# Performance work log

Measured on AMD Instinct MI355X. Metric: run time of the kernel, lower is better.

## Reference

```python
import jax, jax.numpy as jnp
import numpy as np

B, N, DIM = 4, 8192, 512
HEADS, DIM_HEAD = 8, 64
INNER = HEADS * DIM_HEAD          # 512
M = DIM // 2                      # 256 landmarks
PINV_ITERS = 6
RES_K = 33                        # residual depthwise conv kernel (default in NystromAttention)
LN_EPS = 1e-5


def setup_inputs() -> dict:
    key = jax.random.key(0)
    ks = jax.random.split(key, 5)
    s = 0.02
    return {
        "x": jax.random.normal(ks[0], (B, N, DIM), jnp.float32),
        "ln_w": jnp.ones((DIM,), jnp.float32),
        "ln_b": jnp.zeros((DIM,), jnp.float32),
        "w_qkv": jax.random.normal(ks[1], (DIM, 3 * INNER), jnp.float32) * s,
        "w_out": jax.random.normal(ks[2], (INNER, DIM), jnp.float32) * s,
        "b_out": jnp.zeros((DIM,), jnp.float32),
        "res_w": jax.random.normal(ks[3], (HEADS, RES_K), jnp.float32) * s,
    }


def _moore_penrose_pinv(x, iters=PINV_ITERS):
    # Newton-Schulz iteration, exactly as in nystrom-attention
    abs_x = jnp.abs(x)
    col = abs_x.sum(axis=-1)
    row = abs_x.sum(axis=-2)
    z = jnp.swapaxes(x, -1, -2) / (jnp.max(col) * jnp.max(row))
    I = jnp.eye(x.shape[-1], dtype=x.dtype)
    for _ in range(iters):
        xz = x @ z
        z = 0.25 * z @ (13.0 * I - xz @ (15.0 * I - xz @ (7.0 * I - xz)))
    return z


def reference(x, ln_w, ln_b, w_qkv, w_out, b_out, res_w):
    b, n, d = x.shape
    # --- LayerNorm (biased variance, eps=1e-5) ---
    mu = x.mean(-1, keepdims=True)
    var = ((x - mu) ** 2).mean(-1, keepdims=True)
    xn = (x - mu) * jax.lax.rsqrt(var + LN_EPS) * ln_w + ln_b

    # --- pad on the LEFT so seq len divisible by num_landmarks ---
    pad = (-n) % M
    xp = jnp.pad(xn, ((0, 0), (pad, 0), (0, 0)))
    n_p = n + pad

    # --- qkv projection, split heads ---
    qkv = xp @ w_qkv                                  # [b, n_p, 3*inner]
    q, k, v = jnp.split(qkv, 3, axis=-1)
    to_h = lambda t: t.reshape(b, n_p, HEADS, DIM_HEAD).transpose(0, 2, 1, 3)
    q, k, v = to_h(q), to_h(k), to_h(v)               # [b, h, n_p, dh]
    q = q * (DIM_HEAD ** -0.5)

    # --- landmarks: mean over contiguous groups ---
    l = n_p // M
    q_l = q.reshape(b, HEADS, M, l, DIM_HEAD).mean(axis=3)   # [b, h, m, dh]
    k_l = k.reshape(b, HEADS, M, l, DIM_HEAD).mean(axis=3)

    # --- three similarity matrices + softmaxes ---
    sim1 = jnp.einsum('bhnd,bhmd->bhnm', q, k_l)      # [b,h,n_p,m]
    sim2 = jnp.einsum('bhmd,bhld->bhml', q_l, k_l)    # [b,h,m,m]
    sim3 = jnp.einsum('bhmd,bhnd->bhmn', q_l, k)      # [b,h,m,n_p]
    attn1 = jax.nn.softmax(sim1, axis=-1)
    attn2 = jax.nn.softmax(sim2, axis=-1)
    attn3 = jax.nn.softmax(sim3, axis=-1)

    attn2_inv = _moore_penrose_pinv(attn2)
    out = (attn1 @ attn2_inv) @ (attn3 @ v)           # [b,h,n_p,dh]

    # --- residual depthwise conv over sequence dim (groups = heads) ---
    kern = res_w[:, None, :, None]                    # [h, 1, 33, 1] OIHW
    res = jax.lax.conv_general_dilated(
        v, kern, window_strides=(1, 1),
        padding=((RES_K // 2, RES_K // 2), (0, 0)),
        dimension_numbers=('NCHW', 'OIHW', 'NCHW'),
        feature_group_count=HEADS)
    out = out + res

    # --- merge heads, output projection, strip padding, residual add ---
    out = out.transpose(0, 2, 1, 3).reshape(b, n_p, INNER)
    out = out @ w_out + b_out
    out = out[:, -n:]
    return x + out
```

## Files before the change

kernel.cpp:

```cpp
#include <hip/hip_runtime.h>
#include <cstdint>

#define B_ 4
#define N_ 8192
#define DIM_ 512
#define H_ 8
#define DH_ 64
#define M_ 256
#define L_ 32
#define INNER_ 512
#define K3_ 1536
#define RESK_ 33

struct __align__(16) ushort8_t { unsigned short u[8]; };
typedef short bf16x8 __attribute__((ext_vector_type(8)));
typedef float f32x4 __attribute__((ext_vector_type(4)));

__device__ __forceinline__ float bf2f(unsigned short u) {
  return __uint_as_float(((unsigned)u) << 16);
}
__device__ __forceinline__ unsigned short f2bf(float f) {
  unsigned x = __float_as_uint(f);
  return (unsigned short)((x + 0x7fffu + ((x >> 16) & 1u)) >> 16);
}

__global__ __launch_bounds__(256) void ln_bf16(const float* __restrict__ x,
    const float* __restrict__ w, const float* __restrict__ bb, unsigned short* __restrict__ xnb)
{
  int row = blockIdx.x;
  int tid = threadIdx.x;
  float2 v = reinterpret_cast<const float2*>(x + (size_t)row * DIM_)[tid];
  float s = v.x + v.y, s2 = v.x * v.x + v.y * v.y;
  #pragma unroll
  for (int off = 32; off; off >>= 1) { s += __shfl_down(s, off); s2 += __shfl_down(s2, off); }
  __shared__ float rs[4], rs2[4];
  int wid = tid >> 6, lane = tid & 63;
  if (lane == 0) { rs[wid] = s; rs2[wid] = s2; }
  __syncthreads();
  float ts = rs[0] + rs[1] + rs[2] + rs[3];
  float ts2 = rs2[0] + rs2[1] + rs2[2] + rs2[3];
  float mu = ts * (1.f / DIM_);
  float var = ts2 * (1.f / DIM_) - mu * mu;
  float inv = rsqrtf(var + 1e-5f);
  int c = tid * 2;
  unsigned int p0 = f2bf((v.x - mu) * inv * w[c] + bb[c]);
  unsigned int p1 = f2bf((v.y - mu) * inv * w[c + 1] + bb[c + 1]);
  reinterpret_cast<unsigned int*>(xnb + (size_t)row * DIM_)[tid] = p0 | (p1 << 16);
}

__global__ __launch_bounds__(256) void transpose_w(const float* __restrict__ src,
    unsigned short* __restrict__ dst, int K, int C, int qcols, float qs)
{
  __shared__ float T[64][65];
  int c0 = blockIdx.x * 64, k0 = blockIdx.y * 64;
  #pragma unroll 4
  for (int it = 0; it < 16; it++) {
    int idx = it * 256 + threadIdx.x;
    int kk = idx >> 6, cc = idx & 63;
    T[kk][cc] = src[(size_t)(k0 + kk) * C + c0 + cc];
  }
  __syncthreads();
  #pragma unroll 4
  for (int it = 0; it < 16; it++) {
    int idx = it * 256 + threadIdx.x;
    int cc = idx >> 6, kk = idx & 63;
    float v = T[kk][cc];
    int c = c0 + cc;
    dst[(size_t)c * K + k0 + kk] = f2bf(c < qcols ? v * qs : v);
  }
}

__global__ __launch_bounds__(256, 2) void mfma_qkv(const unsigned short* __restrict__ xnb,
    const unsigned short* __restrict__ wT,
    unsigned short* __restrict__ qb, unsigned short* __restrict__ kb, unsigned short* __restrict__ vb)
{
  __shared__ unsigned short As[128][72];
  __shared__ unsigned short Bs[128][72];
  int tid = threadIdx.x;
  int bn = blockIdx.x * 128, bm = blockIdx.y * 128;
  int wid = tid >> 6, lane = tid & 63;
  int wr = wid >> 1, wc = wid & 1;
  int lr = lane & 15, lg = lane >> 4;
  const f32x4 zf = {0.f, 0.f, 0.f, 0.f};
  f32x4 acc[4][4];
  #pragma unroll
  for (int mt = 0; mt < 4; mt++)
    #pragma unroll
    for (int nt = 0; nt < 4; nt++) acc[mt][nt] = zf;

  for (int k0 = 0; k0 < DIM_; k0 += 64) {
    __syncthreads();
    #pragma unroll
    for (int rnd = 0; rnd < 4; rnd++) {
      int idx = rnd * 2048 + tid * 8;
      int row = idx >> 6, col = idx & 63;
      *reinterpret_cast<bf16x8*>(&As[row][col]) =
          *reinterpret_cast<const bf16x8*>(&xnb[(size_t)(bm + row) * DIM_ + k0 + col]);
      *reinterpret_cast<bf16x8*>(&Bs[row][col]) =
          *reinterpret_cast<const bf16x8*>(&wT[(size_t)(bn + row) * DIM_ + k0 + col]);
    }
    __syncthreads();
    bf16x8 af[4][2], bfr[4][2];
    #pragma unroll
    for (int mt = 0; mt < 4; mt++) {
      af[mt][0] = *reinterpret_cast<const bf16x8*>(&As[wr * 64 + mt * 16 + lr][lg * 8]);
      af[mt][1] = *reinterpret_cast<const bf16x8*>(&As[wr * 64 + mt * 16 + lr][32 + lg * 8]);
    }
    #pragma unroll
    for (int nt = 0; nt < 4; nt++) {
      bfr[nt][0] = *reinterpret_cast<const bf16x8*>(&Bs[wc * 64 + nt * 16 + lr][lg * 8]);
      bfr[nt][1] = *reinterpret_cast<const bf16x8*>(&Bs[wc * 64 + nt * 16 + lr][32 + lg * 8]);
    }
    #pragma unroll
    for (int mt = 0; mt < 4; mt++)
      #pragma unroll
      for (int nt = 0; nt < 4; nt++) {
        acc[mt][nt] = __builtin_amdgcn_mfma_f32_16x16x32_bf16(af[mt][0], bfr[nt][0], acc[mt][nt], 0, 0, 0);
        acc[mt][nt] = __builtin_amdgcn_mfma_f32_16x16x32_bf16(af[mt][1], bfr[nt][1], acc[mt][nt], 0, 0, 0);
      }
  }
  #pragma unroll
  for (int nt = 0; nt < 4; nt++) {
    int c = bn + wc * 64 + nt * 16 + lr;
    int which = c >> 9;
    int h = (c >> 6) & (H_ - 1);
    int d = c & 63;
    unsigned short* dst = which == 0 ? qb : (which == 1 ? kb : vb);
    #pragma unroll
    for (int mt = 0; mt < 4; mt++)
      #pragma unroll
      for (int r = 0; r < 4; r++) {
        int row = bm + wr * 64 + mt * 16 + 4 * lg + r;
        int b = row >> 13, n = row & (N_ - 1);
        dst[(((size_t)(b * H_ + h) * N_ + n) << 6) + d] = f2bf(acc[mt][nt][r]);
      }
  }
}

__global__ __launch_bounds__(256, 2) void mfma_out(const unsigned short* __restrict__ oh,
    const unsigned short* __restrict__ wT, const float* __restrict__ bias,
    const float* __restrict__ resid, float* __restrict__ out)
{
  __shared__ unsigned short As[128][72];
  __shared__ unsigned short Bs[128][72];
  int tid = threadIdx.x;
  int bn = blockIdx.x * 128, bm = blockIdx.y * 128;
  int wid = tid >> 6, lane = tid & 63;
  int wr = wid >> 1, wc = wid & 1;
  int lr = lane & 15, lg = lane >> 4;
  const f32x4 zf = {0.f, 0.f, 0.f, 0.f};
  f32x4 acc[4][4];
  #pragma unroll
  for (int mt = 0; mt < 4; mt++)
    #pragma unroll
    for (int nt = 0; nt < 4; nt++) acc[mt][nt] = zf;

  for (int k0 = 0; k0 < INNER_; k0 += 64) {
    __syncthreads();
    #pragma unroll
    for (int rnd = 0; rnd < 4; rnd++) {
      int idx = rnd * 2048 + tid * 8;
      int row = idx >> 6, col = idx & 63;
      *reinterpret_cast<bf16x8*>(&As[row][col]) =
          *reinterpret_cast<const bf16x8*>(&oh[((size_t)(bm + row) << 9) + k0 + col]);
      *reinterpret_cast<bf16x8*>(&Bs[row][col]) =
          *reinterpret_cast<const bf16x8*>(&wT[(size_t)(bn + row) * INNER_ + k0 + col]);
    }
    __syncthreads();
    bf16x8 af[4][2], bfr[4][2];
    #pragma unroll
    for (int mt = 0; mt < 4; mt++) {
      af[mt][0] = *reinterpret_cast<const bf16x8*>(&As[wr * 64 + mt * 16 + lr][lg * 8]);
      af[mt][1] = *reinterpret_cast<const bf16x8*>(&As[wr * 64 + mt * 16 + lr][32 + lg * 8]);
    }
    #pragma unroll
    for (int nt = 0; nt < 4; nt++) {
      bfr[nt][0] = *reinterpret_cast<const bf16x8*>(&Bs[wc * 64 + nt * 16 + lr][lg * 8]);
      bfr[nt][1] = *reinterpret_cast<const bf16x8*>(&Bs[wc * 64 + nt * 16 + lr][32 + lg * 8]);
    }
    #pragma unroll
    for (int mt = 0; mt < 4; mt++)
      #pragma unroll
      for (int nt = 0; nt < 4; nt++) {
        acc[mt][nt] = __builtin_amdgcn_mfma_f32_16x16x32_bf16(af[mt][0], bfr[nt][0], acc[mt][nt], 0, 0, 0);
        acc[mt][nt] = __builtin_amdgcn_mfma_f32_16x16x32_bf16(af[mt][1], bfr[nt][1], acc[mt][nt], 0, 0, 0);
      }
  }
  #pragma unroll
  for (int nt = 0; nt < 4; nt++) {
    int c = bn + wc * 64 + nt * 16 + lr;
    float bias_c = bias[c];
    #pragma unroll
    for (int mt = 0; mt < 4; mt++)
      #pragma unroll
      for (int r = 0; r < 4; r++) {
        int row = bm + wr * 64 + mt * 16 + 4 * lg + r;
        out[(size_t)row * DIM_ + c] = acc[mt][nt][r] + bias_c + resid[(size_t)row * DIM_ + c];
      }
  }
}

__global__ __launch_bounds__(64) void landmark_kernel(const unsigned short* __restrict__ qb,
    const unsigned short* __restrict__ kb, float* __restrict__ ql, float* __restrict__ kl,
    unsigned short* __restrict__ qlb, unsigned short* __restrict__ klb)
{
  int id = blockIdx.x;
  int m = id & (M_ - 1);
  int bh = id >> 8;
  int d = threadIdx.x;
  size_t base = (((size_t)bh * N_ + m * L_) << 6) + d;
  float sq = 0, sk = 0;
  #pragma unroll 4
  for (int j = 0; j < L_; j++) {
    sq += bf2f(qb[base + ((size_t)j << 6)]);
    sk += bf2f(kb[base + ((size_t)j << 6)]);
  }
  float qv = sq * (1.f / L_);
  float kv = sk * (1.f / L_);
  size_t o = ((size_t)bh * M_ + m) * DH_ + d;
  ql[o] = qv;
  kl[o] = kv;
  qlb[o] = f2bf(qv);
  klb[o] = f2bf(kv);
}

__global__ __launch_bounds__(256) void attn2_kernel(const float* __restrict__ ql,
    const float* __restrict__ kl, float* __restrict__ a2, unsigned short* __restrict__ a2b)
{
  int id = blockIdx.x;
  int i = id & (M_ - 1);
  int bh = id >> 8;
  int j = threadIdx.x;
  __shared__ float qs[DH_];
  __shared__ float wred[4];
  if (j < DH_) qs[j] = ql[((size_t)bh * M_ + i) * DH_ + j];
  __syncthreads();
  const float* krow = kl + ((size_t)bh * M_ + j) * DH_;
  float s = 0;
  #pragma unroll
  for (int d = 0; d < DH_; d++) s += qs[d] * krow[d];
  float mx = s;
  #pragma unroll
  for (int off = 1; off < 64; off <<= 1) mx = fmaxf(mx, __shfl_xor(mx, off));
  int wid = j >> 6, lane = j & 63;
  if (lane == 0) wred[wid] = mx;
  __syncthreads();
  mx = fmaxf(fmaxf(wred[0], wred[1]), fmaxf(wred[2], wred[3]));
  float e = __expf(s - mx);
  float sum = e;
  #pragma unroll
  for (int off = 1; off < 64; off <<= 1) sum += __shfl_xor(sum, off);
  __syncthreads();
  if (lane == 0) wred[wid] = sum;
  __syncthreads();
  sum = wred[0] + wred[1] + wred[2] + wred[3];
  float p = e / sum;
  size_t o = ((size_t)bh * M_ + i) * M_ + j;
  a2[o] = p;
  a2b[o] = f2bf(p);
}

__global__ void zero_scal(unsigned int* scal) { scal[threadIdx.x] = 0u; }

__global__ __launch_bounds__(256) void pinv_scale_kernel(const float* __restrict__ a2,
    unsigned int* __restrict__ scal)
{
  int bh = blockIdx.x;
  int t = threadIdx.x;
  const float* xb = a2 + (size_t)bh * M_ * M_;
  float rowsum = 0, colsum = 0;
  for (int j = 0; j < M_; j++) {
    rowsum += xb[(size_t)t * M_ + j];
    colsum += xb[(size_t)j * M_ + t];
  }
  #pragma unroll
  for (int off = 1; off < 64; off <<= 1) {
    rowsum = fmaxf(rowsum, __shfl_xor(rowsum, off));
    colsum = fmaxf(colsum, __shfl_xor(colsum, off));
  }
  __shared__ float wr[4], wc[4];
  int wid = t >> 6, lane = t & 63;
  if (lane == 0) { wr[wid] = rowsum; wc[wid] = colsum; }
  __syncthreads();
  if (t == 0) {
    float rm = fmaxf(fmaxf(wr[0], wr[1]), fmaxf(wr[2], wr[3]));
    float cm = fmaxf(fmaxf(wc[0], wc[1]), fmaxf(wc[2], wc[3]));
    atomicMax(&scal[0], __float_as_uint(rm));
    atomicMax(&scal[1], __float_as_uint(cm));
  }
}

__global__ __launch_bounds__(256) void zinit_kernel(const float* __restrict__ a2,
    const unsigned int* __restrict__ scal,
    unsigned short* __restrict__ zR, unsigned short* __restrict__ zT)
{
  __shared__ float T[64][65];
  int j0 = blockIdx.x * 64, i0 = blockIdx.y * 64;
  size_t bb = (size_t)blockIdx.z * (M_ * M_);
  float inv = 1.f / (__uint_as_float(scal[0]) * __uint_as_float(scal[1]));
  int tid = threadIdx.x;
  #pragma unroll 4
  for (int pass = 0; pass < 16; pass++) {
    int idx = pass * 256 + tid;
    int ii = idx >> 6, jj = idx & 63;
    float v = a2[bb + (size_t)(i0 + ii) * M_ + j0 + jj];
    T[ii][jj] = v;
    zT[bb + (size_t)(i0 + ii) * M_ + j0 + jj] = f2bf(v * inv);
  }
  __syncthreads();
  #pragma unroll 4
  for (int pass = 0; pass < 16; pass++) {
    int idx = pass * 256 + tid;
    int jj = idx >> 6, ii = idx & 63;
    zR[bb + (size_t)(j0 + jj) * M_ + i0 + ii] = f2bf(T[ii][jj] * inv);
  }
}

__global__ __launch_bounds__(256, 2) void bgemm_ns(
    const unsigned short* __restrict__ Ab, const unsigned short* __restrict__ BTb,
    unsigned short* __restrict__ Rb, unsigned short* __restrict__ YTb,
    float aY, float sY, float sR)
{
  __shared__ unsigned short Ash[64][72];
  __shared__ unsigned short Bsh[64][72];
  int bn = blockIdx.x * 64, bm = blockIdx.y * 64;
  size_t bb = (size_t)blockIdx.z * (M_ * M_);
  int tid = threadIdx.x, wid = tid >> 6, lane = tid & 63;
  int lr = lane & 15, lg = lane >> 4;
  int wr = (wid >> 1) * 32, wc = (wid & 1) * 32;
  const f32x4 zf = {0.f, 0.f, 0.f, 0.f};
  f32x4 acc[2][2];
  #pragma unroll
  for (int mt = 0; mt < 2; mt++)
    #pragma unroll
    for (int nt = 0; nt < 2; nt++) acc[mt][nt] = zf;

  for (int k0 = 0; k0 < M_; k0 += 64) {
    __syncthreads();
    #pragma unroll
    for (int pass = 0; pass < 2; pass++) {
      int idx = pass * 2048 + tid * 8;
      int row = idx >> 6, col = idx & 63;
      *reinterpret_cast<bf16x8*>(&Ash[row][col]) =
          *reinterpret_cast<const bf16x8*>(&Ab[bb + (size_t)(bm + row) * M_ + k0 + col]);
      *reinterpret_cast<bf16x8*>(&Bsh[row][col]) =
          *reinterpret_cast<const bf16x8*>(&BTb[bb + (size_t)(bn + row) * M_ + k0 + col]);
    }
    __syncthreads();
    #pragma unroll
    for (int kk = 0; kk < 64; kk += 32) {
      bf16x8 a0 = *reinterpret_cast<const bf16x8*>(&Ash[wr + lr][kk + lg * 8]);
      bf16x8 a1 = *reinterpret_cast<const bf16x8*>(&Ash[wr + 16 + lr][kk + lg * 8]);
      bf16x8 b0 = *reinterpret_cast<const bf16x8*>(&Bsh[wc + lr][kk + lg * 8]);
      bf16x8 b1 = *reinterpret_cast<const bf16x8*>(&Bsh[wc + 16 + lr][kk + lg * 8]);
      acc[0][0] = __builtin_amdgcn_mfma_f32_16x16x32_bf16(a0, b0, acc[0][0], 0, 0, 0);
      acc[0][1] = __builtin_amdgcn_mfma_f32_16x16x32_bf16(a0, b1, acc[0][1], 0, 0, 0);
      acc[1][0] = __builtin_amdgcn_mfma_f32_16x16x32_bf16(a1, b0, acc[1][0], 0, 0, 0);
      acc[1][1] = __builtin_amdgcn_mfma_f32_16x16x32_bf16(a1, b1, acc[1][1], 0, 0, 0);
    }
  }
  if (Rb) {
    #pragma unroll
    for (int mt = 0; mt < 2; mt++)
      #pragma unroll
      for (int nt = 0; nt < 2; nt++) {
        int col = bn + wc + nt * 16 + lr;
        #pragma unroll
        for (int r = 0; r < 4; r++) {
          int row = bm + wr + mt * 16 + 4 * lg + r;
          Rb[bb + (size_t)row * M_ + col] = f2bf(sR * acc[mt][nt][r]);
        }
      }
  }
  if (YTb) {
    __syncthreads();
    #pragma unroll
    for (int mt = 0; mt < 2; mt++)
      #pragma unroll
      for (int nt = 0; nt < 2; nt++) {
        int nl = wc + nt * 16 + lr;
        #pragma unroll
        for (int r = 0; r < 4; r++) {
          int ml = wr + mt * 16 + 4 * lg + r;
          float t = sY * acc[mt][nt][r] + ((bm + ml) == (bn + nl) ? aY : 0.f);
          Ash[nl][ml] = f2bf(t);
        }
      }
    __syncthreads();
    #pragma unroll
    for (int pass = 0; pass < 2; pass++) {
      int idx = pass * 2048 + tid * 8;
      int nl = idx >> 6, ml = idx & 63;
      *reinterpret_cast<bf16x8*>(&YTb[bb + (size_t)(bn + nl) * M_ + bm + ml]) =
          *reinterpret_cast<const bf16x8*>(&Ash[nl][ml]);
    }
  }
}

__global__ __launch_bounds__(256) void gemm_w2(
    const unsigned short* __restrict__ zR,
    const unsigned short* __restrict__ pvT, unsigned short* __restrict__ w2t)
{
  int bm = blockIdx.x * 64;
  int batch = blockIdx.y;
  size_t bz = (size_t)batch * (M_ * M_);
  size_t bp = (size_t)batch << 14;
  int tid = threadIdx.x, wid = tid >> 6, lane = tid & 63;
  int lr = lane & 15, lg = lane >> 4;
  int r0 = bm + wid * 16;
  const f32x4 zf = {0.f, 0.f, 0.f, 0.f};
  f32x4 acc[4];
  #pragma unroll
  for (int nt = 0; nt < 4; nt++) acc[nt] = zf;

  #pragma unroll
  for (int k0 = 0; k0 < M_; k0 += 32) {
    bf16x8 a = *reinterpret_cast<const bf16x8*>(&zR[bz + (size_t)(r0 + lr) * M_ + k0 + lg * 8]);
    #pragma unroll
    for (int nt = 0; nt < 4; nt++) {
      bf16x8 b = *reinterpret_cast<const bf16x8*>(&pvT[bp + (size_t)(nt * 16 + lr) * M_ + k0 + lg * 8]);
      acc[nt] = __builtin_amdgcn_mfma_f32_16x16x32_bf16(a, b, acc[nt], 0, 0, 0);
    }
  }
  #pragma unroll
  for (int nt = 0; nt < 4; nt++) {
    int col = nt * 16 + lr;
    #pragma unroll
    for (int r = 0; r < 4; r++) {
      int row = r0 + 4 * lg + r;
      w2t[bp + (size_t)col * M_ + row] = f2bf(acc[nt][r]);
    }
  }
}

__global__ __launch_bounds__(512) void pv_mfma(
    const unsigned short* __restrict__ kb, const unsigned short* __restrict__ vb,
    const unsigned short* __restrict__ qlb,
    float* __restrict__ pvpart, float2* __restrict__ msbuf)
{
  int slice = blockIdx.x;
  int bh    = blockIdx.z;
  int tid = threadIdx.x, wid = tid >> 6, lane = tid & 63;
  int lr = lane & 15, lg = lane >> 4;

  __shared__ unsigned short klds[64][72];
  __shared__ unsigned short vtld[64][72];
  __shared__ unsigned short plds_all[8][32][72];
  unsigned short (*plds)[72] = plds_all[wid];

  int mbase = wid * 32;
  const unsigned short* qbase = qlb + (((size_t)bh * M_ + mbase) << 6);
  bf16x8 qf[2][2];
  #pragma unroll
  for (int rt = 0; rt < 2; rt++)
    #pragma unroll
    for (int h2 = 0; h2 < 2; h2++)
      qf[rt][h2] = *reinterpret_cast<const bf16x8*>(&qbase[((rt * 16 + lr) << 6) + h2 * 32 + lg * 8]);

  const f32x4 zf = {0.f, 0.f, 0.f, 0.f};
  f32x4 oacc[2][4];
  #pragma unroll
  for (int rt = 0; rt < 2; rt++)
    #pragma unroll
    for (int dt = 0; dt < 4; dt++) oacc[rt][dt] = zf;
  float mrun[8], srun[8];
  #pragma unroll
  for (int i = 0; i < 8; i++) { mrun[i] = -1e30f; srun[i] = 0.f; }

  const unsigned short* kgb = kb + (((size_t)bh * N_ + slice * 1024) << 6);
  const unsigned short* vgb = vb + (((size_t)bh * N_ + slice * 1024) << 6);

  for (int c = 0; c < 16; c++) {
    __syncthreads();
    {
      int key = tid >> 3, seg = tid & 7;
      size_t goff = (((size_t)(c * 64 + key)) << 6) + seg * 8;
      bf16x8 kv = *reinterpret_cast<const bf16x8*>(&kgb[goff]);
      *reinterpret_cast<bf16x8*>(&klds[key][seg * 8]) = kv;
      bf16x8 vv = *reinterpret_cast<const bf16x8*>(&vgb[goff]);
      int col = key ^ (seg << 3);
      #pragma unroll
      for (int j = 0; j < 8; j++) vtld[seg * 8 + j][col] = (unsigned short)vv[j];
    }
    __syncthreads();
    f32x4 sacc[2][4];
    #pragma unroll
    for (int rt = 0; rt < 2; rt++)
      #pragma unroll
      for (int ct = 0; ct < 4; ct++) {
        bf16x8 b0 = *reinterpret_cast<const bf16x8*>(&klds[ct * 16 + lr][lg * 8]);
        bf16x8 b1 = *reinterpret_cast<const bf16x8*>(&klds[ct * 16 + lr][32 + lg * 8]);
        f32x4 a = __builtin_amdgcn_mfma_f32_16x16x32_bf16(qf[rt][0], b0, zf, 0, 0, 0);
        sacc[rt][ct] = __builtin_amdgcn_mfma_f32_16x16x32_bf16(qf[rt][1], b1, a, 0, 0, 0);
      }
    #pragma unroll
    for (int rt = 0; rt < 2; rt++)
      #pragma unroll
      for (int r = 0; r < 4; r++) {
        int ri = rt * 4 + r;
        float mc = fmaxf(fmaxf(sacc[rt][0][r], sacc[rt][1][r]), fmaxf(sacc[rt][2][r], sacc[rt][3][r]));
        #pragma unroll
        for (int off = 1; off < 16; off <<= 1) mc = fmaxf(mc, __shfl_xor(mc, off));
        float mnew = fmaxf(mrun[ri], mc);
        float corr = __expf(mrun[ri] - mnew);
        float psum = 0.f;
        #pragma unroll
        for (int ct = 0; ct < 4; ct++) {
          float p = __expf(sacc[rt][ct][r] - mnew);
          sacc[rt][ct][r] = p;
          psum += p;
        }
        #pragma unroll
        for (int off = 1; off < 16; off <<= 1) psum += __shfl_xor(psum, off);
        srun[ri] = srun[ri] * corr + psum;
        mrun[ri] = mnew;
        #pragma unroll
        for (int dt = 0; dt < 4; dt++) oacc[rt][dt][r] *= corr;
        #pragma unroll
        for (int ct = 0; ct < 4; ct++)
          plds[rt * 16 + 4 * lg + r][ct * 16 + lr] = f2bf(sacc[rt][ct][r]);
      }
    __builtin_amdgcn_s_waitcnt(0);
    bf16x8 pa[2][2];
    #pragma unroll
    for (int rt = 0; rt < 2; rt++)
      #pragma unroll
      for (int h = 0; h < 2; h++)
        pa[rt][h] = *reinterpret_cast<const bf16x8*>(&plds[rt * 16 + lr][h * 32 + lg * 8]);
    #pragma unroll
    for (int dt = 0; dt < 4; dt++) {
      int d = dt * 16 + lr;
      bf16x8 bv0 = *reinterpret_cast<const bf16x8*>(&vtld[d][(lg * 8) ^ (d & 0x38)]);
      bf16x8 bv1 = *reinterpret_cast<const bf16x8*>(&vtld[d][(32 + lg * 8) ^ (d & 0x38)]);
      #pragma unroll
      for (int rt = 0; rt < 2; rt++) {
        oacc[rt][dt] = __builtin_amdgcn_mfma_f32_16x16x32_bf16(pa[rt][0], bv0, oacc[rt][dt], 0, 0, 0);
        oacc[rt][dt] = __builtin_amdgcn_mfma_f32_16x16x32_bf16(pa[rt][1], bv1, oacc[rt][dt], 0, 0, 0);
      }
    }
  }
  size_t pbase = (((size_t)(bh * 8 + slice) * M_ + mbase) << 6);
  #pragma unroll
  for (int rt = 0; rt < 2; rt++)
    #pragma unroll
    for (int dt = 0; dt < 4; dt++)
      #pragma unroll
      for (int r = 0; r < 4; r++)
        pvpart[pbase + ((size_t)(rt * 16 + 4 * lg + r) << 6) + dt * 16 + lr] = oacc[rt][dt][r];
  if (lr == 0) {
    #pragma unroll
    for (int rt = 0; rt < 2; rt++)
      #pragma unroll
      for (int r = 0; r < 4; r++)
        msbuf[(size_t)(bh * 8 + slice) * M_ + mbase + rt * 16 + 4 * lg + r] =
            make_float2(mrun[rt * 4 + r], srun[rt * 4 + r]);
  }
}

__global__ __launch_bounds__(256) void pv_combine(const float* __restrict__ pvpart,
    const float2* __restrict__ msbuf, unsigned short* __restrict__ pvT)
{
  int row = blockIdx.x * 4 + (threadIdx.x >> 6);
  int bh = row >> 8, m = row & (M_ - 1);
  int d = threadIdx.x & 63;
  float2 ms[8];
  float mg = -1e30f;
  #pragma unroll
  for (int s = 0; s < 8; s++) {
    ms[s] = msbuf[(size_t)(bh * 8 + s) * M_ + m];
    mg = fmaxf(mg, ms[s].x);
  }
  float ssum = 0.f, o = 0.f;
  #pragma unroll
  for (int s = 0; s < 8; s++) {
    float w = __expf(ms[s].x - mg);
    ssum += ms[s].y * w;
    o += w * pvpart[(((size_t)(bh * 8 + s) * M_ + m) << 6) + d];
  }
  pvT[((size_t)bh << 14) + (size_t)d * M_ + m] = f2bf(o / ssum);
}

__global__ __launch_bounds__(256) void attn1_kernel(
    const unsigned short* __restrict__ qb,
    const unsigned short* __restrict__ klb,
    const unsigned short* __restrict__ w2t,
    unsigned short* __restrict__ oh)
{
  int ntile = blockIdx.x & 31;
  int bh = blockIdx.x >> 5;
  int h = bh & (H_ - 1), b = bh >> 3;
  int tid = threadIdx.x, wid = tid >> 6, lane = tid & 63;
  int lr = lane & 15, lg = lane >> 4;
  __shared__ unsigned short klds[256][72];
  __shared__ unsigned short plds_all[4][16][264];
  unsigned short* plds = &plds_all[wid][0][0];

  const unsigned short* qbh  = qb  + (((size_t)bh * N_) << 6);
  const unsigned short* klbh = klb + ((size_t)bh << 14);
  const unsigned short* w2bh = w2t + ((size_t)bh << 14);

  #pragma unroll
  for (int e = 0; e < 8; e++) {
    int idx = e * 2048 + tid * 8;
    int row = idx >> 6, col = idx & 63;
    *reinterpret_cast<bf16x8*>(&klds[row][col]) =
        *reinterpret_cast<const bf16x8*>(&klbh[((size_t)row << 6) + col]);
  }
  __syncthreads();

  const f32x4 zf = {0.f, 0.f, 0.f, 0.f};
  for (int sub = 0; sub < 4; sub++) {
    int n0 = ntile * 256 + sub * 64 + wid * 16;
    bf16x8 aq0 = *reinterpret_cast<const bf16x8*>(&qbh[((size_t)(n0 + lr) << 6) + lg * 8]);
    bf16x8 aq1 = *reinterpret_cast<const bf16x8*>(&qbh[((size_t)(n0 + lr) << 6) + 32 + lg * 8]);
    f32x4 accs[16];
    #pragma unroll
    for (int mt = 0; mt < 16; mt++) {
      bf16x8 b0 = *reinterpret_cast<const bf16x8*>(&klds[mt * 16 + lr][lg * 8]);
      bf16x8 b1 = *reinterpret_cast<const bf16x8*>(&klds[mt * 16 + lr][32 + lg * 8]);
      f32x4 a = __builtin_amdgcn_mfma_f32_16x16x32_bf16(aq0, b0, zf, 0, 0, 0);
      accs[mt] = __builtin_amdgcn_mfma_f32_16x16x32_bf16(aq1, b1, a, 0, 0, 0);
    }
    float rs[4];
    #pragma unroll
    for (int r = 0; r < 4; r++) {
      float m0 = accs[0][r];
      #pragma unroll
      for (int mt = 1; mt < 16; mt++) m0 = fmaxf(m0, accs[mt][r]);
      #pragma unroll
      for (int off = 1; off < 16; off <<= 1) m0 = fmaxf(m0, __shfl_xor(m0, off));
      float s0 = 0.f;
      #pragma unroll
      for (int mt = 0; mt < 16; mt++) {
        float p = __expf(accs[mt][r] - m0);
        accs[mt][r] = p;
        s0 += p;
      }
      #pragma unroll
      for (int off = 1; off < 16; off <<= 1) s0 += __shfl_xor(s0, off);
      rs[r] = 1.f / s0;
    }
    #pragma unroll
    for (int mt = 0; mt < 16; mt++)
      #pragma unroll
      for (int r = 0; r < 4; r++)
        plds[(4 * lg + r) * 264 + mt * 16 + lr] = f2bf(accs[mt][r]);
    __builtin_amdgcn_s_waitcnt(0);
    bf16x8 pa[8];
    #pragma unroll
    for (int mc = 0; mc < 8; mc++)
      pa[mc] = *reinterpret_cast<const bf16x8*>(&plds[lr * 264 + mc * 32 + lg * 8]);
    f32x4 acco[4];
    #pragma unroll
    for (int dt = 0; dt < 4; dt++) {
      f32x4 a = zf;
      #pragma unroll
      for (int mc = 0; mc < 8; mc++) {
        bf16x8 wf = *reinterpret_cast<const bf16x8*>(&w2bh[(size_t)(dt * 16 + lr) * M_ + mc * 32 + lg * 8]);
        a = __builtin_amdgcn_mfma_f32_16x16x32_bf16(pa[mc], wf, a, 0, 0, 0);
      }
      acco[dt] = a;
    }
    #pragma unroll
    for (int dt = 0; dt < 4; dt++)
      #pragma unroll
      for (int r = 0; r < 4; r++) {
        int n = n0 + 4 * lg + r;
        oh[((size_t)(b * N_ + n) << 9) + h * DH_ + dt * 16 + lr] = f2bf(acco[dt][r] * rs[r]);
      }
  }
}

__global__ __launch_bounds__(256) void conv_kernel(const unsigned short* __restrict__ vb,
    const float* __restrict__ rw, unsigned short* __restrict__ oh)
{
  int bh = blockIdx.y;
  int h = bh & (H_ - 1), b = bh >> 3;
  int d = threadIdx.x & 63, g = threadIdx.x >> 6;
  int n0 = blockIdx.x * 128 + g * 32;
  const unsigned short* vbb = vb + (((size_t)bh * N_) << 6) + d;
  float w[64];
  #pragma unroll
  for (int j = 0; j < 64; j++) {
    int nn = n0 - 16 + j;
    w[j] = (nn >= 0 && nn < N_) ? bf2f(vbb[(size_t)nn << 6]) : 0.f;
  }
  float rwr[RESK_];
  #pragma unroll
  for (int j = 0; j < RESK_; j++) rwr[j] = rw[h * RESK_ + j];
  size_t obase = (((size_t)(b * N_ + n0)) << 9) + h * 64 + d;
  #pragma unroll
  for (int t = 0; t < 32; t++) {
    float acc = 0.f;
    #pragma unroll
    for (int j = 0; j < RESK_; j++) acc += rwr[j] * w[t + j];
    size_t oi = obase + ((size_t)t << 9);
    oh[oi] = f2bf(bf2f(oh[oi]) + acc);
  }
}

extern "C" void kernel_launch(void* const* d_in, const int* in_sizes, int n_in,
                              void* d_out, int out_size, void* d_ws, size_t ws_size,
                              hipStream_t stream)
{
  const float* x     = (const float*)d_in[0];
  const float* ln_w  = (const float*)d_in[1];
  const float* ln_b  = (const float*)d_in[2];
  const float* w_qkv = (const float*)d_in[3];
  const float* w_out = (const float*)d_in[4];
  const float* b_out = (const float*)d_in[5];
  const float* res_w = (const float*)d_in[6];
  float* out = (float*)d_out;

  const size_t HEADEL = (size_t)B_ * H_ * N_ * DH_;
  const size_t SMALL  = (size_t)B_ * H_ * M_ * DH_;
  const size_t MSQ    = (size_t)B_ * H_ * M_ * M_;

  char* p = (char*)d_ws;
  auto alloc = [&](size_t bytes) { char* r = p; p += (bytes + 255) & ~(size_t)255; return r; };

  unsigned short* qb  = (unsigned short*)alloc(HEADEL * 2);
  unsigned short* kb  = (unsigned short*)alloc(HEADEL * 2);
  unsigned short* vb  = (unsigned short*)alloc(HEADEL * 2);
  unsigned short* oh  = (unsigned short*)alloc(HEADEL * 2);
  char* unA = alloc(HEADEL * 2);
  unsigned short* xnb = (unsigned short*)unA;
  unsigned short* z0R = (unsigned short*)unA;
  unsigned short* z0T = z0R + MSQ;
  unsigned short* z1R = z0T + MSQ;
  unsigned short* z1T = z1R + MSQ;
  char* unB = alloc(HEADEL * 2);
  float*  pvpart = (float*)unB;
  float2* msbuf  = (float2*)(unB + (size_t)B_ * H_ * 8 * M_ * DH_ * 4);
  unsigned short* ub  = (unsigned short*)unB;
  unsigned short* vTb = ub + MSQ;
  unsigned short* wTb = vTb + MSQ;
  unsigned short* yTb = wTb + MSQ;

  unsigned short* wqkvT = (unsigned short*)alloc((size_t)K3_ * DIM_ * 2);
  unsigned short* woutT = (unsigned short*)alloc((size_t)DIM_ * INNER_ * 2);
  float* ql  = (float*)alloc(SMALL * 4);
  float* kl  = (float*)alloc(SMALL * 4);
  unsigned short* qlb = (unsigned short*)alloc(SMALL * 2);
  unsigned short* klb = (unsigned short*)alloc(SMALL * 2);
  unsigned short* pvT = (unsigned short*)alloc(SMALL * 2);
  unsigned short* w2t = (unsigned short*)alloc(SMALL * 2);
  unsigned short* a2b = (unsigned short*)alloc(MSQ * 2);
  unsigned int* scal  = (unsigned int*)alloc(256);
  if ((size_t)(p - (char*)d_ws) > ws_size) return;

  float* a2 = (float*)d_out;

  ln_bf16<<<B_ * N_, 256, 0, stream>>>(x, ln_w, ln_b, xnb);
  transpose_w<<<dim3(K3_ / 64, DIM_ / 64), 256, 0, stream>>>(w_qkv, wqkvT, DIM_, K3_, INNER_, 0.125f);
  transpose_w<<<dim3(DIM_ / 64, INNER_ / 64), 256, 0, stream>>>(w_out, woutT, INNER_, DIM_, 0, 1.f);
  mfma_qkv<<<dim3(K3_ / 128, (B_ * N_) / 128), 256, 0, stream>>>(xnb, wqkvT, qb, kb, vb);
  landmark_kernel<<<B_ * H_ * M_, 64, 0, stream>>>(qb, kb, ql, kl, qlb, klb);
  attn2_kernel<<<B_ * H_ * M_, 256, 0, stream>>>(ql, kl, a2, a2b);
  zero_scal<<<1, 2, 0, stream>>>(scal);
  pinv_scale_kernel<<<B_ * H_, 256, 0, stream>>>(a2, scal);
  pv_mfma<<<dim3(8, 1, B_ * H_), 512, 0, stream>>>(kb, vb, qlb, pvpart, msbuf);
  pv_combine<<<(B_ * H_ * M_) / 4, 256, 0, stream>>>(pvpart, msbuf, pvT);
  zinit_kernel<<<dim3(4, 4, B_ * H_), 256, 0, stream>>>(a2, scal, z0R, z0T);

  unsigned short *cR = z0R, *cT = z0T, *nR = z1R, *nT = z1T;
  dim3 g44(4, 4, B_ * H_);
  for (int it = 0; it < 6; it++) {
    bgemm_ns<<<g44, 256, 0, stream>>>(a2b, cT, ub, vTb, 7.f, -1.f, 1.f);
    bgemm_ns<<<g44, 256, 0, stream>>>(ub, vTb, nullptr, wTb, 15.f, -1.f, 0.f);
    bgemm_ns<<<g44, 256, 0, stream>>>(ub, wTb, nullptr, yTb, 13.f, -1.f, 0.f);
    bgemm_ns<<<g44, 256, 0, stream>>>(cR, yTb, nR, nT, 0.f, 0.25f, 0.25f);
    unsigned short* t;
    t = cR; cR = nR; nR = t;  t = cT; cT = nT; nT = t;
  }

  gemm_w2<<<dim3(4, B_ * H_), 256, 0, stream>>>(cR, pvT, w2t);

  attn1_kernel<<<B_ * H_ * (N_ / 256), 256, 0, stream>>>(qb, klb, w2t, oh);
  conv_kernel<<<dim3(N_ / 128, B_ * H_), 256, 0, stream>>>(vb, res_w, oh);
  mfma_out<<<dim3(DIM_ / 128, (B_ * N_) / 128), 256, 0, stream>>>(oh, woutT, b_out, x, out);
}
```

Measured before the change: 663.5 us.

## Fuse Newton-Schulz z-update with next xz product via algebraic reuse; swizzle GEMM tiles

Removes one batched GEMM launch per Newton-Schulz iteration. Since x·z_new = 0.25·(x·z)·Y = 0.25·u·Y, one combined kernel computes both z_new = 0.25·z·Y and the next u-derived matrix (7I - 0.25·u·Y) in a single launch over a doubled grid. Also adds a workgroup-ID swizzle to the QKV and output GEMMs for cache locality, and raises wave priority around the MFMA blocks. The reformulation changes the rounding path, since u is now built from bf16 products of previous u rather than recomputed from x·z, so error may accumulate across iterations.

```diff
diff --git a/kernel.cpp b/kernel.cpp
--- a/kernel.cpp
+++ b/kernel.cpp
@@ -77,7 +77,10 @@
   __shared__ unsigned short As[128][72];
   __shared__ unsigned short Bs[128][72];
   int tid = threadIdx.x;
-  int bn = blockIdx.x * 128, bm = blockIdx.y * 128;
+  int nwgx = gridDim.x, nwg = nwgx * gridDim.y;
+  int l = blockIdx.y * nwgx + blockIdx.x;
+  int swz = (l & 7) * (nwg >> 3) + (l >> 3);
+  int bn = (swz % nwgx) * 128, bm = (swz / nwgx) * 128;
   int wid = tid >> 6, lane = tid & 63;
   int wr = wid >> 1, wc = wid & 1;
   int lr = lane & 15, lg = lane >> 4;
@@ -111,6 +114,7 @@
       bfr[nt][0] = *reinterpret_cast<const bf16x8*>(&Bs[wc * 64 + nt * 16 + lr][lg * 8]);
       bfr[nt][1] = *reinterpret_cast<const bf16x8*>(&Bs[wc * 64 + nt * 16 + lr][32 + lg * 8]);
     }
+    __builtin_amdgcn_s_setprio(1);
     #pragma unroll
     for (int mt = 0; mt < 4; mt++)
       #pragma unroll
@@ -118,6 +122,7 @@
         acc[mt][nt] = __builtin_amdgcn_mfma_f32_16x16x32_bf16(af[mt][0], bfr[nt][0], acc[mt][nt], 0, 0, 0);
         acc[mt][nt] = __builtin_amdgcn_mfma_f32_16x16x32_bf16(af[mt][1], bfr[nt][1], acc[mt][nt], 0, 0, 0);
       }
+    __builtin_amdgcn_s_setprio(0);
   }
   #pragma unroll
   for (int nt = 0; nt < 4; nt++) {
@@ -144,7 +149,10 @@
   __shared__ unsigned short As[128][72];
   __shared__ unsigned short Bs[128][72];
   int tid = threadIdx.x;
-  int bn = blockIdx.x * 128, bm = blockIdx.y * 128;
+  int nwgx = gridDim.x, nwg = nwgx * gridDim.y;
+  int l = blockIdx.y * nwgx + blockIdx.x;
+  int swz = (l & 7) * (nwg >> 3) + (l >> 3);
+  int bn = (swz % nwgx) * 128, bm = (swz / nwgx) * 128;
   int wid = tid >> 6, lane = tid & 63;
   int wr = wid >> 1, wc = wid & 1;
   int lr = lane & 15, lg = lane >> 4;
@@ -178,6 +186,7 @@
       bfr[nt][0] = *reinterpret_cast<const bf16x8*>(&Bs[wc * 64 + nt * 16 + lr][lg * 8]);
       bfr[nt][1] = *reinterpret_cast<const bf16x8*>(&Bs[wc * 64 + nt * 16 + lr][32 + lg * 8]);
     }
+    __builtin_amdgcn_s_setprio(1);
     #pragma unroll
     for (int mt = 0; mt < 4; mt++)
       #pragma unroll
@@ -185,6 +194,7 @@
         acc[mt][nt] = __builtin_amdgcn_mfma_f32_16x16x32_bf16(af[mt][0], bfr[nt][0], acc[mt][nt], 0, 0, 0);
         acc[mt][nt] = __builtin_amdgcn_mfma_f32_16x16x32_bf16(af[mt][1], bfr[nt][1], acc[mt][nt], 0, 0, 0);
       }
+    __builtin_amdgcn_s_setprio(0);
   }
   #pragma unroll
   for (int nt = 0; nt < 4; nt++) {
@@ -392,6 +402,91 @@
       int idx = pass * 2048 + tid * 8;
       int nl = idx >> 6, ml = idx & 63;
       *reinterpret_cast<bf16x8*>(&YTb[bb + (size_t)(bn + nl) * M_ + bm + ml]) =
+          *reinterpret_cast<const bf16x8*>(&Ash[nl][ml]);
+    }
+  }
+}
+
+__global__ __launch_bounds__(256, 2) void bgemm_ns2(
+    const unsigned short* __restrict__ Az, const unsigned short* __restrict__ Au,
+    const unsigned short* __restrict__ BTb,
+    unsigned short* __restrict__ Rz, unsigned short* __restrict__ Ru,
+    unsigned short* __restrict__ YTb, int split)
+{
+  __shared__ unsigned short Ash[64][72];
+  __shared__ unsigned short Bsh[64][72];
+  int ysel = (int)blockIdx.y >= split;
+  const unsigned short* Ab = ysel ? Au : Az;
+  unsigned short* Rb = ysel ? Ru : Rz;
+  unsigned short* Yb = ysel ? YTb : nullptr;
+  int bn = blockIdx.x * 64;
+  int bm = ((int)blockIdx.y - (ysel ? split : 0)) * 64;
+  size_t bb = (size_t)blockIdx.z * (M_ * M_);
+  int tid = threadIdx.x, wid = tid >> 6, lane = tid & 63;
+  int lr = lane & 15, lg = lane >> 4;
+  int wr = (wid >> 1) * 32, wc = (wid & 1) * 32;
+  const f32x4 zf = {0.f, 0.f, 0.f, 0.f};
+  f32x4 acc[2][2];
+  #pragma unroll
+  for (int mt = 0; mt < 2; mt++)
+    #pragma unroll
+    for (int nt = 0; nt < 2; nt++) acc[mt][nt] = zf;
+
+  for (int k0 = 0; k0 < M_; k0 += 64) {
+    __syncthreads();
+    #pragma unroll
+    for (int pass = 0; pass < 2; pass++) {
+      int idx = pass * 2048 + tid * 8;
+      int row = idx >> 6, col = idx & 63;
+      *reinterpret_cast<bf16x8*>(&Ash[row][col]) =
+          *reinterpret_cast<const bf16x8*>(&Ab[bb + (size_t)(bm + row) * M_ + k0 + col]);
+      *reinterpret_cast<bf16x8*>(&Bsh[row][col]) =
+          *reinterpret_cast<const bf16x8*>(&BTb[bb + (size_t)(bn + row) * M_ + k0 + col]);
+    }
+    __syncthreads();
+    #pragma unroll
+    for (int kk = 0; kk < 64; kk += 32) {
+      bf16x8 a0 = *reinterpret_cast<const bf16x8*>(&Ash[wr + lr][kk + lg * 8]);
+      bf16x8 a1 = *reinterpret_cast<const bf16x8*>(&Ash[wr + 16 + lr][kk + lg * 8]);
+      bf16x8 b0 = *reinterpret_cast<const bf16x8*>(&Bsh[wc + lr][kk + lg * 8]);
+      bf16x8 b1 = *reinterpret_cast<const bf16x8*>(&Bsh[wc + 16 + lr][kk + lg * 8]);
+      acc[0][0] = __builtin_amdgcn_mfma_f32_16x16x32_bf16(a0, b0, acc[0][0], 0, 0, 0);
+      acc[0][1] = __builtin_amdgcn_mfma_f32_16x16x32_bf16(a0, b1, acc[0][1], 0, 0, 0);
+      acc[1][0] = __builtin_amdgcn_mfma_f32_16x16x32_bf16(a1, b0, acc[1][0], 0, 0, 0);
+      acc[1][1] = __builtin_amdgcn_mfma_f32_16x16x32_bf16(a1, b1, acc[1][1], 0, 0, 0);
+    }
+  }
+  #pragma unroll
+  for (int mt = 0; mt < 2; mt++)
+    #pragma unroll
+    for (int nt = 0; nt < 2; nt++) {
+      int col = bn + wc + nt * 16 + lr;
+      #pragma unroll
+      for (int r = 0; r < 4; r++) {
+        int row = bm + wr + mt * 16 + 4 * lg + r;
+        Rb[bb + (size_t)row * M_ + col] = f2bf(0.25f * acc[mt][nt][r]);
+      }
+    }
+  if (Yb) {
+    __syncthreads();
+    #pragma unroll
+    for (int mt = 0; mt < 2; mt++)
+      #pragma unroll
+      for (int nt = 0; nt < 2; nt++) {
+        int nl = wc + nt * 16 + lr;
+        #pragma unroll
+        for (int r = 0; r < 4; r++) {
+          int ml = wr + mt * 16 + 4 * lg + r;
+          float t = -0.25f * acc[mt][nt][r] + ((bm + ml) == (bn + nl) ? 7.f : 0.f);
+          Ash[nl][ml] = f2bf(t);
+        }
+      }
+    __syncthreads();
+    #pragma unroll
+    for (int pass = 0; pass < 2; pass++) {
+      int idx = pass * 2048 + tid * 8;
+      int nl = idx >> 6, ml = idx & 63;
+      *reinterpret_cast<bf16x8*>(&Yb[bb + (size_t)(bn + nl) * M_ + bm + ml]) =
           *reinterpret_cast<const bf16x8*>(&Ash[nl][ml]);
     }
   }
@@ -614,6 +709,7 @@
     bf16x8 aq0 = *reinterpret_cast<const bf16x8*>(&qbh[((size_t)(n0 + lr) << 6) + lg * 8]);
     bf16x8 aq1 = *reinterpret_cast<const bf16x8*>(&qbh[((size_t)(n0 + lr) << 6) + 32 + lg * 8]);
     f32x4 accs[16];
+    __builtin_amdgcn_s_setprio(1);
     #pragma unroll
     for (int mt = 0; mt < 16; mt++) {
       bf16x8 b0 = *reinterpret_cast<const bf16x8*>(&klds[mt * 16 + lr][lg * 8]);
@@ -621,6 +717,7 @@
       f32x4 a = __builtin_amdgcn_mfma_f32_16x16x32_bf16(aq0, b0, zf, 0, 0, 0);
       accs[mt] = __builtin_amdgcn_mfma_f32_16x16x32_bf16(aq1, b1, a, 0, 0, 0);
     }
+    __builtin_amdgcn_s_setprio(0);
     float rs[4];
     #pragma unroll
     for (int r = 0; r < 4; r++) {
@@ -651,6 +748,7 @@
     for (int mc = 0; mc < 8; mc++)
       pa[mc] = *reinterpret_cast<const bf16x8*>(&plds[lr * 264 + mc * 32 + lg * 8]);
     f32x4 acco[4];
+    __builtin_amdgcn_s_setprio(1);
     #pragma unroll
     for (int dt = 0; dt < 4; dt++) {
       f32x4 a = zf;
@@ -661,6 +759,7 @@
       }
       acco[dt] = a;
     }
+    __builtin_amdgcn_s_setprio(0);
     #pragma unroll
     for (int dt = 0; dt < 4; dt++)
       #pragma unroll
@@ -728,7 +827,7 @@
   unsigned short* z0R = (unsigned short*)unA;
   unsigned short* z0T = z0R + MSQ;
   unsigned short* z1R = z0T + MSQ;
-  unsigned short* z1T = z1R + MSQ;
+  unsigned short* u2  = z1R + MSQ;
   char* unB = alloc(HEADEL * 2);
   float*  pvpart = (float*)unB;
   float2* msbuf  = (float2*)(unB + (size_t)B_ * H_ * 8 * M_ * DH_ * 4);
@@ -763,15 +862,21 @@
   pv_combine<<<(B_ * H_ * M_) / 4, 256, 0, stream>>>(pvpart, msbuf, pvT);
   zinit_kernel<<<dim3(4, 4, B_ * H_), 256, 0, stream>>>(a2, scal, z0R, z0T);
 
-  unsigned short *cR = z0R, *cT = z0T, *nR = z1R, *nT = z1T;
   dim3 g44(4, 4, B_ * H_);
+  dim3 g48(4, 8, B_ * H_);
+  bgemm_ns<<<g44, 256, 0, stream>>>(a2b, z0T, ub, vTb, 7.f, -1.f, 1.f);
+  unsigned short *cR = z0R, *nR = z1R, *cu = ub, *nu = u2;
   for (int it = 0; it < 6; it++) {
-    bgemm_ns<<<g44, 256, 0, stream>>>(a2b, cT, ub, vTb, 7.f, -1.f, 1.f);
-    bgemm_ns<<<g44, 256, 0, stream>>>(ub, vTb, nullptr, wTb, 15.f, -1.f, 0.f);
-    bgemm_ns<<<g44, 256, 0, stream>>>(ub, wTb, nullptr, yTb, 13.f, -1.f, 0.f);
-    bgemm_ns<<<g44, 256, 0, stream>>>(cR, yTb, nR, nT, 0.f, 0.25f, 0.25f);
-    unsigned short* t;
-    t = cR; cR = nR; nR = t;  t = cT; cT = nT; nT = t;
+    bgemm_ns<<<g44, 256, 0, stream>>>(cu, vTb, nullptr, wTb, 15.f, -1.f, 0.f);
+    bgemm_ns<<<g44, 256, 0, stream>>>(cu, wTb, nullptr, yTb, 13.f, -1.f, 0.f);
+    if (it < 5) {
+      bgemm_ns2<<<g48, 256, 0, stream>>>(cR, cu, yTb, nR, nu, vTb, 4);
+      unsigned short* t;
+      t = cR; cR = nR; nR = t;  t = cu; cu = nu; nu = t;
+    } else {
+      bgemm_ns2<<<g44, 256, 0, stream>>>(cR, cu, yTb, nR, nu, vTb, 4);
+      cR = nR;
+    }
   }
 
   gemm_w2<<<dim3(4, B_ * H_), 256, 0, stream>>>(cR, pvT, w2t);
```

Measured after the change: 608.6 us. 1.09x faster.
